# Optimization experiments

Hardware: AMD Instinct MI355X
Metric: run time of the kernel (lower is better)

The kernel has to match this reference:

```python
import jax, jax.numpy as jnp
import numpy as np

HIDDEN = 2048
INTER = 768
NUM_EXPERTS = 32
TOP_K = 8
B, S = 1, 512


def setup_inputs() -> dict:
    key = jax.random.key(0)
    ks = jax.random.split(key, 5)
    scale_h = 1.0 / np.sqrt(HIDDEN)
    scale_i = 1.0 / np.sqrt(INTER)
    return {
        "hidden_states": jax.random.normal(ks[0], (B, S, HIDDEN), dtype=jnp.float32),
        # router gate: nn.Linear(hidden, num_experts), weight [E, H]
        "gate_w": jax.random.normal(ks[1], (NUM_EXPERTS, HIDDEN), dtype=jnp.float32) * scale_h,
        # stacked expert weights, already transposed for x @ W as in setup_tt: [E, H, I] / [E, I, H]
        "gate_proj": jax.random.normal(ks[2], (NUM_EXPERTS, HIDDEN, INTER), dtype=jnp.float32) * scale_h,
        "up_proj": jax.random.normal(ks[3], (NUM_EXPERTS, HIDDEN, INTER), dtype=jnp.float32) * scale_h,
        "down_proj": jax.random.normal(ks[4], (NUM_EXPERTS, INTER, HIDDEN), dtype=jnp.float32) * scale_i,
    }


def reference(hidden_states, gate_w, gate_proj, up_proj, down_proj):
    b, s, h = hidden_states.shape
    x = hidden_states.reshape(-1, h)                      # [T, H]
    t = x.shape[0]

    # --- routing: softmax over experts -> top-k -> renormalize (norm_topk_prob=True) ---
    router_logits = x @ gate_w.T                          # [T, E]
    probs = jax.nn.softmax(router_logits, axis=-1)
    top_w, top_i = jax.lax.top_k(probs, TOP_K)            # [T, K]
    top_w = top_w / jnp.sum(top_w, axis=-1, keepdims=True)

    # dense combine weights [T, E]; top-k indices are distinct per token
    comb = jnp.zeros((t, NUM_EXPERTS), dtype=x.dtype)
    comb = comb.at[jnp.arange(t)[:, None], top_i].add(top_w)

    # --- expert GLU MLPs (all experts, combine-masked; same math as dispatch/combine) ---
    g = jnp.einsum('th,ehi->eti', x, gate_proj)           # [E, T, I]
    u = jnp.einsum('th,ehi->eti', x, up_proj)             # [E, T, I]
    glu = jax.nn.silu(g) * u                              # [E, T, I]
    o = jnp.einsum('eti,eih->eth', glu, down_proj)        # [E, T, H]

    # weighted combine over experts
    y = jnp.einsum('eth,te->th', o, comb)                 # [T, H]
    return y.reshape(b, s, h)
```

## Files before the change

### kernel.cpp

```cpp
#include <hip/hip_runtime.h>
#include <math.h>

#define H 2048
#define I 768
#define NE 32
#define TOPK 8
#define T 512

typedef __attribute__((ext_vector_type(4))) float f32x4;
typedef __attribute__((ext_vector_type(8))) short s16x8;

#define WS_TOPW_OFF    1024
#define WS_ENTRIES_OFF (1024 + 16384)
#define WS_XB_OFF      131072
#define WS_GLU_OFF     (4*1024*1024)

__device__ __forceinline__ unsigned int f2bf(float f) {
    unsigned int u = __float_as_uint(f);
    return (u + 0x7FFFu + ((u >> 16) & 1u)) >> 16;
}

__global__ __launch_bounds__(256) void convert_x_kernel(
    const float* __restrict__ x, ushort* __restrict__ xb)
{
    int i = (blockIdx.x * 256 + threadIdx.x) * 8;
    float4 a = *(const float4*)(x + i);
    float4 b = *(const float4*)(x + i + 4);
    uint4 o;
    o.x = f2bf(a.x) | (f2bf(a.y) << 16);
    o.y = f2bf(a.z) | (f2bf(a.w) << 16);
    o.z = f2bf(b.x) | (f2bf(b.y) << 16);
    o.w = f2bf(b.z) | (f2bf(b.w) << 16);
    *(uint4*)(xb + i) = o;
}

__global__ __launch_bounds__(256) void router_kernel(
    const float* __restrict__ x, const float* __restrict__ gw,
    float* __restrict__ topw, int* __restrict__ counts, int* __restrict__ entries)
{
    int t = blockIdx.x;
    const float* xt = x + (size_t)t * H;
    __shared__ float logits[NE];

    int e   = threadIdx.x >> 3;
    int sub = threadIdx.x & 7;
    const float* we = gw + (size_t)e * H;
    float acc = 0.f;
    for (int h = sub; h < H; h += 8) acc += xt[h] * we[h];
    acc += __shfl_down(acc, 4);
    acc += __shfl_down(acc, 2);
    acc += __shfl_down(acc, 1);
    if (sub == 0) logits[e] = acc;
    __syncthreads();

    if (threadIdx.x == 0) {
        float l[NE];
        #pragma unroll
        for (int i2 = 0; i2 < NE; ++i2) l[i2] = logits[i2];
        int bi[TOPK]; float bv[TOPK];
        for (int k = 0; k < TOPK; ++k) {
            float best = -1e30f; int b = 0;
            for (int i2 = 0; i2 < NE; ++i2)
                if (l[i2] > best) { best = l[i2]; b = i2; }
            bi[k] = b; bv[k] = best; l[b] = -1e30f;
        }
        float m = bv[0], s = 0.f, w[TOPK];
        for (int k = 0; k < TOPK; ++k) { w[k] = expf(bv[k] - m); s += w[k]; }
        float inv = 1.f / s;
        for (int k = 0; k < TOPK; ++k) {
            int p = t * TOPK + k;
            topw[p] = w[k] * inv;
            int pos = atomicAdd(&counts[bi[k]], 1);
            entries[bi[k] * T + pos] = p;
        }
    }
}

__global__ __launch_bounds__(256) void gateup_kernel(
    const ushort* __restrict__ xb, const float* __restrict__ Wg, const float* __restrict__ Wu,
    const int* __restrict__ counts, const int* __restrict__ entries,
    ushort* __restrict__ glu)
{
    int e  = blockIdx.x;
    int nt = blockIdx.y;
    int mt = blockIdx.z;
    int n  = counts[e];
    if (mt * 128 >= n) return;

    __shared__ ushort A_lds[128 * 72];
    __shared__ ushort Bg_lds[64 * 72];
    __shared__ ushort Bu_lds[64 * 72];
    __shared__ int prow[128];

    int tid = threadIdx.x;
    if (tid < 128) {
        int idx = mt * 128 + tid;
        prow[tid] = (idx < n) ? entries[e * T + idx] : -1;
    }
    __syncthreads();

    int lane = tid & 63;
    int wid  = tid >> 6;
    int wm = wid >> 1, wn = wid & 1;
    int quad = lane >> 4, l16 = lane & 15;

    f32x4 accg[4][2], accu[4][2];
    #pragma unroll
    for (int mi = 0; mi < 4; ++mi)
        #pragma unroll
        for (int ni = 0; ni < 2; ++ni) {
            #pragma unroll
            for (int r = 0; r < 4; ++r) { accg[mi][ni][r] = 0.f; accu[mi][ni][r] = 0.f; }
        }

    const float* wgB = Wg + (size_t)e * H * I + nt * 64;
    const float* wuB = Wu + (size_t)e * H * I + nt * 64;
    int n4 = tid & 15;
    int kb = tid >> 4;

    for (int hc = 0; hc < H; hc += 64) {
        #pragma unroll
        for (int s = 0; s < 4; ++s) {
            int c = tid + s * 256;
            int r = c >> 3, ch = c & 7;
            int p = prow[r];
            int4 v = make_int4(0, 0, 0, 0);
            if (p >= 0)
                v = *(const int4*)(xb + (size_t)(p >> 3) * H + hc + ch * 8);
            *(int4*)&A_lds[r * 72 + ch * 8] = v;
        }
        #pragma unroll
        for (int q = 0; q < 2; ++q) {
            int k = kb * 2 + q * 32;
            const float* g0 = wgB + (size_t)(hc + k) * I + n4 * 4;
            const float* u0 = wuB + (size_t)(hc + k) * I + n4 * 4;
            float4 ga = *(const float4*)g0;
            float4 gb = *(const float4*)(g0 + I);
            float4 ua = *(const float4*)u0;
            float4 ub = *(const float4*)(u0 + I);
            float gax[4] = {ga.x, ga.y, ga.z, ga.w};
            float gbx[4] = {gb.x, gb.y, gb.z, gb.w};
            float uax[4] = {ua.x, ua.y, ua.z, ua.w};
            float ubx[4] = {ub.x, ub.y, ub.z, ub.w};
            #pragma unroll
            for (int i2 = 0; i2 < 4; ++i2) {
                *(unsigned int*)&Bg_lds[(n4 * 4 + i2) * 72 + k] = f2bf(gax[i2]) | (f2bf(gbx[i2]) << 16);
                *(unsigned int*)&Bu_lds[(n4 * 4 + i2) * 72 + k] = f2bf(uax[i2]) | (f2bf(ubx[i2]) << 16);
            }
        }
        __syncthreads();
        #pragma unroll
        for (int s = 0; s < 2; ++s) {
            int ko = s * 32 + quad * 8;
            s16x8 af[4];
            #pragma unroll
            for (int mi = 0; mi < 4; ++mi)
                af[mi] = *(const s16x8*)&A_lds[(wm * 64 + mi * 16 + l16) * 72 + ko];
            #pragma unroll
            for (int ni = 0; ni < 2; ++ni) {
                s16x8 bg = *(const s16x8*)&Bg_lds[(wn * 32 + ni * 16 + l16) * 72 + ko];
                s16x8 bu = *(const s16x8*)&Bu_lds[(wn * 32 + ni * 16 + l16) * 72 + ko];
                #pragma unroll
                for (int mi = 0; mi < 4; ++mi) {
                    accg[mi][ni] = __builtin_amdgcn_mfma_f32_16x16x32_bf16(af[mi], bg, accg[mi][ni], 0, 0, 0);
                    accu[mi][ni] = __builtin_amdgcn_mfma_f32_16x16x32_bf16(af[mi], bu, accu[mi][ni], 0, 0, 0);
                }
            }
        }
        __syncthreads();
    }

    #pragma unroll
    for (int mi = 0; mi < 4; ++mi) {
        #pragma unroll
        for (int reg = 0; reg < 4; ++reg) {
            int r = wm * 64 + mi * 16 + quad * 4 + reg;
            int p = prow[r];
            if (p >= 0) {
                size_t base = (size_t)p * I + nt * 64 + wn * 32;
                #pragma unroll
                for (int ni = 0; ni < 2; ++ni) {
                    float g = accg[mi][ni][reg];
                    float u = accu[mi][ni][reg];
                    float sv = g / (1.f + __expf(-g)) * u;
                    glu[base + ni * 16 + l16] = (ushort)f2bf(sv);
                }
            }
        }
    }
}

__global__ __launch_bounds__(256) void down_kernel(
    const ushort* __restrict__ glu, const float* __restrict__ Wd,
    const int* __restrict__ counts, const int* __restrict__ entries,
    const float* __restrict__ topw, float* __restrict__ out)
{
    int e  = blockIdx.x;
    int nt = blockIdx.y;
    int mt = blockIdx.z;
    int n  = counts[e];
    if (mt * 128 >= n) return;

    __shared__ ushort A_lds[128 * 72];
    __shared__ ushort B_lds[64 * 72];
    __shared__ int   prow[128];
    __shared__ float pw[128];

    int tid = threadIdx.x;
    if (tid < 128) {
        int idx = mt * 128 + tid;
        int p = (idx < n) ? entries[e * T + idx] : -1;
        prow[tid] = p;
        pw[tid]   = (p >= 0) ? topw[p] : 0.f;
    }
    __syncthreads();

    int lane = tid & 63;
    int wid  = tid >> 6;
    int wm = wid >> 1, wn = wid & 1;
    int quad = lane >> 4, l16 = lane & 15;

    f32x4 acc[4][2];
    #pragma unroll
    for (int mi = 0; mi < 4; ++mi)
        #pragma unroll
        for (int ni = 0; ni < 2; ++ni) {
            #pragma unroll
            for (int r = 0; r < 4; ++r) acc[mi][ni][r] = 0.f;
        }

    const float* wdB = Wd + (size_t)e * I * H + nt * 64;
    int n4 = tid & 15;
    int kb = tid >> 4;

    for (int kc = 0; kc < I; kc += 64) {
        #pragma unroll
        for (int s = 0; s < 4; ++s) {
            int c = tid + s * 256;
            int r = c >> 3, ch = c & 7;
            int p = prow[r];
            int4 v = make_int4(0, 0, 0, 0);
            if (p >= 0)
                v = *(const int4*)(glu + (size_t)p * I + kc + ch * 8);
            *(int4*)&A_lds[r * 72 + ch * 8] = v;
        }
        #pragma unroll
        for (int q = 0; q < 2; ++q) {
            int k = kb * 2 + q * 32;
            const float* d0 = wdB + (size_t)(kc + k) * H + n4 * 4;
            float4 da = *(const float4*)d0;
            float4 db = *(const float4*)(d0 + H);
            float dax[4] = {da.x, da.y, da.z, da.w};
            float dbx[4] = {db.x, db.y, db.z, db.w};
            #pragma unroll
            for (int i2 = 0; i2 < 4; ++i2)
                *(unsigned int*)&B_lds[(n4 * 4 + i2) * 72 + k] = f2bf(dax[i2]) | (f2bf(dbx[i2]) << 16);
        }
        __syncthreads();
        #pragma unroll
        for (int s = 0; s < 2; ++s) {
            int ko = s * 32 + quad * 8;
            s16x8 af[4];
            #pragma unroll
            for (int mi = 0; mi < 4; ++mi)
                af[mi] = *(const s16x8*)&A_lds[(wm * 64 + mi * 16 + l16) * 72 + ko];
            #pragma unroll
            for (int ni = 0; ni < 2; ++ni) {
                s16x8 bf = *(const s16x8*)&B_lds[(wn * 32 + ni * 16 + l16) * 72 + ko];
                #pragma unroll
                for (int mi = 0; mi < 4; ++mi)
                    acc[mi][ni] = __builtin_amdgcn_mfma_f32_16x16x32_bf16(af[mi], bf, acc[mi][ni], 0, 0, 0);
            }
        }
        __syncthreads();
    }

    #pragma unroll
    for (int mi = 0; mi < 4; ++mi) {
        #pragma unroll
        for (int reg = 0; reg < 4; ++reg) {
            int r = wm * 64 + mi * 16 + quad * 4 + reg;
            int p = prow[r];
            if (p >= 0) {
                int tok = p >> 3;
                float wgt = pw[r];
                size_t base = (size_t)tok * H + nt * 64 + wn * 32;
                #pragma unroll
                for (int ni = 0; ni < 2; ++ni)
                    atomicAdd(&out[base + ni * 16 + l16], wgt * acc[mi][ni][reg]);
            }
        }
    }
}

extern "C" void kernel_launch(void* const* d_in, const int* in_sizes, int n_in,
                              void* d_out, int out_size, void* d_ws, size_t ws_size,
                              hipStream_t stream) {
    const float* x  = (const float*)d_in[0];
    const float* gw = (const float*)d_in[1];
    const float* Wg = (const float*)d_in[2];
    const float* Wu = (const float*)d_in[3];
    const float* Wd = (const float*)d_in[4];
    float* out = (float*)d_out;

    char* ws = (char*)d_ws;
    int*    counts  = (int*)ws;
    float*  topw    = (float*)(ws + WS_TOPW_OFF);
    int*    entries = (int*)(ws + WS_ENTRIES_OFF);
    ushort* xb      = (ushort*)(ws + WS_XB_OFF);
    ushort* glu     = (ushort*)(ws + WS_GLU_OFF);

    hipMemsetAsync(d_ws, 0, 1024, stream);
    hipMemsetAsync(d_out, 0, (size_t)out_size * sizeof(float), stream);

    convert_x_kernel<<<T * H / (256 * 8), 256, 0, stream>>>(x, xb);
    router_kernel<<<T, 256, 0, stream>>>(x, gw, topw, counts, entries);

    dim3 g2(NE, I / 64, 4);
    gateup_kernel<<<g2, 256, 0, stream>>>(xb, Wg, Wu, counts, entries, glu);

    dim3 g3(NE, H / 64, 4);
    down_kernel<<<g3, 256, 0, stream>>>(glu, Wd, counts, entries, topw, out);
}
```

Baseline: 684.8 us.

## Software-pipeline expert GEMMs with async global-to-LDS loads and double-buffered A

After: 686.5 us. About the same (+0.3%).

```diff
diff --git a/kernel.cpp b/kernel.cpp
--- a/kernel.cpp
+++ b/kernel.cpp
@@ -18,6 +18,11 @@
 __device__ __forceinline__ unsigned int f2bf(float f) {
     unsigned int u = __float_as_uint(f);
     return (u + 0x7FFFu + ((u >> 16) & 1u)) >> 16;
+}
+__device__ __forceinline__ unsigned int cvtpk(float lo, float hi) {
+    unsigned int r;
+    asm("v_cvt_pk_bf16_f32 %0, %1, %2" : "=v"(r) : "v"(lo), "v"(hi));
+    return r;
 }
 
 __global__ __launch_bounds__(256) void convert_x_kernel(
@@ -27,10 +32,10 @@
     float4 a = *(const float4*)(x + i);
     float4 b = *(const float4*)(x + i + 4);
     uint4 o;
-    o.x = f2bf(a.x) | (f2bf(a.y) << 16);
-    o.y = f2bf(a.z) | (f2bf(a.w) << 16);
-    o.z = f2bf(b.x) | (f2bf(b.y) << 16);
-    o.w = f2bf(b.z) | (f2bf(b.w) << 16);
+    o.x = cvtpk(a.x, a.y);
+    o.y = cvtpk(a.z, a.w);
+    o.z = cvtpk(b.x, b.y);
+    o.w = cvtpk(b.z, b.w);
     *(uint4*)(xb + i) = o;
 }
 
@@ -87,7 +92,7 @@
     int n  = counts[e];
     if (mt * 128 >= n) return;
 
-    __shared__ ushort A_lds[128 * 72];
+    __shared__ ushort A_lds[2][128 * 64];
     __shared__ ushort Bg_lds[64 * 72];
     __shared__ ushort Bu_lds[64 * 72];
     __shared__ int prow[128];
@@ -104,6 +109,44 @@
     int wm = wid >> 1, wn = wid & 1;
     int quad = lane >> 4, l16 = lane & 15;
 
+    const ushort* asrc[4];
+    #pragma unroll
+    for (int j = 0; j < 4; ++j) {
+        int r = (wid * 4 + j) * 8 + (lane >> 3);
+        int c = (lane & 7) ^ (r & 7);
+        int p = prow[r]; if (p < 0) p = 0;
+        asrc[j] = xb + (size_t)(p >> 3) * H + c * 8;
+    }
+
+    int n4 = tid & 15, kb = tid >> 4;
+    const float* pg = Wg + (size_t)e * H * I + (size_t)(kb * 2) * I + nt * 64 + n4 * 4;
+    const float* pu = Wu + (size_t)e * H * I + (size_t)(kb * 2) * I + nt * 64 + n4 * 4;
+    float4 bg[2][2], bu[2][2];
+
+    int bofs[2][4];
+    #pragma unroll
+    for (int q = 0; q < 2; ++q)
+        #pragma unroll
+        for (int i2 = 0; i2 < 4; ++i2) {
+            int r = n4 * 4 + i2, d = kb + 16 * q;
+            bofs[q][i2] = r * 72 + (((d >> 2) ^ ((r >> 3) & 7)) << 3) + ((d & 3) << 1);
+        }
+    int aofs[2][4], brofs[2][2];
+    #pragma unroll
+    for (int s = 0; s < 2; ++s) {
+        int g = 4 * s + quad;
+        #pragma unroll
+        for (int mi = 0; mi < 4; ++mi) {
+            int R = wm * 64 + mi * 16 + l16;
+            aofs[s][mi] = R * 64 + ((g ^ (R & 7)) << 3);
+        }
+        #pragma unroll
+        for (int ni = 0; ni < 2; ++ni) {
+            int R = wn * 32 + ni * 16 + l16;
+            brofs[s][ni] = R * 72 + ((g ^ ((R >> 3) & 7)) << 3);
+        }
+    }
+
     f32x4 accg[4][2], accu[4][2];
     #pragma unroll
     for (int mi = 0; mi < 4; ++mi)
@@ -113,61 +156,67 @@
             for (int r = 0; r < 4; ++r) { accg[mi][ni][r] = 0.f; accu[mi][ni][r] = 0.f; }
         }
 
-    const float* wgB = Wg + (size_t)e * H * I + nt * 64;
-    const float* wuB = Wu + (size_t)e * H * I + nt * 64;
-    int n4 = tid & 15;
-    int kb = tid >> 4;
-
-    for (int hc = 0; hc < H; hc += 64) {
-        #pragma unroll
-        for (int s = 0; s < 4; ++s) {
-            int c = tid + s * 256;
-            int r = c >> 3, ch = c & 7;
-            int p = prow[r];
-            int4 v = make_int4(0, 0, 0, 0);
-            if (p >= 0)
-                v = *(const int4*)(xb + (size_t)(p >> 3) * H + hc + ch * 8);
-            *(int4*)&A_lds[r * 72 + ch * 8] = v;
-        }
+    auto issue_a = [&](int bi2, int hc) {
+        #pragma unroll
+        for (int j = 0; j < 4; ++j)
+            __builtin_amdgcn_global_load_lds(
+                (const __attribute__((address_space(1))) void*)(asrc[j] + hc),
+                (__attribute__((address_space(3))) void*)(&A_lds[bi2][(wid * 4 + j) * 512]),
+                16, 0, 0);
+    };
+    auto load_b = [&]() {
         #pragma unroll
         for (int q = 0; q < 2; ++q) {
-            int k = kb * 2 + q * 32;
-            const float* g0 = wgB + (size_t)(hc + k) * I + n4 * 4;
-            const float* u0 = wuB + (size_t)(hc + k) * I + n4 * 4;
-            float4 ga = *(const float4*)g0;
-            float4 gb = *(const float4*)(g0 + I);
-            float4 ua = *(const float4*)u0;
-            float4 ub = *(const float4*)(u0 + I);
-            float gax[4] = {ga.x, ga.y, ga.z, ga.w};
-            float gbx[4] = {gb.x, gb.y, gb.z, gb.w};
-            float uax[4] = {ua.x, ua.y, ua.z, ua.w};
-            float ubx[4] = {ub.x, ub.y, ub.z, ub.w};
+            const float* g0 = pg + (size_t)(32 * q) * I;
+            const float* u0 = pu + (size_t)(32 * q) * I;
+            bg[q][0] = *(const float4*)g0; bg[q][1] = *(const float4*)(g0 + I);
+            bu[q][0] = *(const float4*)u0; bu[q][1] = *(const float4*)(u0 + I);
+        }
+        pg += 64 * I; pu += 64 * I;
+    };
+    auto store_b = [&]() {
+        #pragma unroll
+        for (int q = 0; q < 2; ++q) {
+            const float* gl = (const float*)&bg[q][0];
+            const float* gh = (const float*)&bg[q][1];
+            const float* ul = (const float*)&bu[q][0];
+            const float* uh = (const float*)&bu[q][1];
             #pragma unroll
             for (int i2 = 0; i2 < 4; ++i2) {
-                *(unsigned int*)&Bg_lds[(n4 * 4 + i2) * 72 + k] = f2bf(gax[i2]) | (f2bf(gbx[i2]) << 16);
-                *(unsigned int*)&Bu_lds[(n4 * 4 + i2) * 72 + k] = f2bf(uax[i2]) | (f2bf(ubx[i2]) << 16);
+                *(unsigned int*)&Bg_lds[bofs[q][i2]] = cvtpk(gl[i2], gh[i2]);
+                *(unsigned int*)&Bu_lds[bofs[q][i2]] = cvtpk(ul[i2], uh[i2]);
             }
         }
-        __syncthreads();
+    };
+
+    issue_a(0, 0);
+    load_b();
+
+    for (int it = 0; it < H / 64; ++it) {
+        __builtin_amdgcn_s_barrier();
+        if (it + 1 < H / 64) issue_a((it + 1) & 1, (it + 1) * 64);
+        store_b();
+        if (it + 1 < H / 64) load_b();
+        asm volatile("s_waitcnt lgkmcnt(0) vmcnt(12)" ::: "memory");
+        __builtin_amdgcn_sched_barrier(0);
+        __builtin_amdgcn_s_barrier();
+        const ushort* Ab = A_lds[it & 1];
         #pragma unroll
         for (int s = 0; s < 2; ++s) {
-            int ko = s * 32 + quad * 8;
             s16x8 af[4];
             #pragma unroll
-            for (int mi = 0; mi < 4; ++mi)
-                af[mi] = *(const s16x8*)&A_lds[(wm * 64 + mi * 16 + l16) * 72 + ko];
+            for (int mi = 0; mi < 4; ++mi) af[mi] = *(const s16x8*)&Ab[aofs[s][mi]];
             #pragma unroll
             for (int ni = 0; ni < 2; ++ni) {
-                s16x8 bg = *(const s16x8*)&Bg_lds[(wn * 32 + ni * 16 + l16) * 72 + ko];
-                s16x8 bu = *(const s16x8*)&Bu_lds[(wn * 32 + ni * 16 + l16) * 72 + ko];
+                s16x8 bgf  = *(const s16x8*)&Bg_lds[brofs[s][ni]];
+                s16x8 buf2 = *(const s16x8*)&Bu_lds[brofs[s][ni]];
                 #pragma unroll
                 for (int mi = 0; mi < 4; ++mi) {
-                    accg[mi][ni] = __builtin_amdgcn_mfma_f32_16x16x32_bf16(af[mi], bg, accg[mi][ni], 0, 0, 0);
-                    accu[mi][ni] = __builtin_amdgcn_mfma_f32_16x16x32_bf16(af[mi], bu, accu[mi][ni], 0, 0, 0);
+                    accg[mi][ni] = __builtin_amdgcn_mfma_f32_16x16x32_bf16(af[mi], bgf,  accg[mi][ni], 0, 0, 0);
+                    accu[mi][ni] = __builtin_amdgcn_mfma_f32_16x16x32_bf16(af[mi], buf2, accu[mi][ni], 0, 0, 0);
                 }
             }
         }
-        __syncthreads();
     }
 
     #pragma unroll
@@ -201,8 +250,8 @@
     int n  = counts[e];
     if (mt * 128 >= n) return;
 
-    __shared__ ushort A_lds[128 * 72];
-    __shared__ ushort B_lds[64 * 72];
+    __shared__ ushort A_lds[2][128 * 64];
+    __shared__ ushort Bd_lds[64 * 72];
     __shared__ int   prow[128];
     __shared__ float pw[128];
 
@@ -220,6 +269,43 @@
     int wm = wid >> 1, wn = wid & 1;
     int quad = lane >> 4, l16 = lane & 15;
 
+    const ushort* asrc[4];
+    #pragma unroll
+    for (int j = 0; j < 4; ++j) {
+        int r = (wid * 4 + j) * 8 + (lane >> 3);
+        int c = (lane & 7) ^ (r & 7);
+        int p = prow[r]; if (p < 0) p = 0;
+        asrc[j] = glu + (size_t)p * I + c * 8;
+    }
+
+    int n4 = tid & 15, kb = tid >> 4;
+    const float* pd = Wd + (size_t)e * I * H + (size_t)(kb * 2) * H + nt * 64 + n4 * 4;
+    float4 bd[2][2];
+
+    int bofs[2][4];
+    #pragma unroll
+    for (int q = 0; q < 2; ++q)
+        #pragma unroll
+        for (int i2 = 0; i2 < 4; ++i2) {
+            int r = n4 * 4 + i2, d = kb + 16 * q;
+            bofs[q][i2] = r * 72 + (((d >> 2) ^ ((r >> 3) & 7)) << 3) + ((d & 3) << 1);
+        }
+    int aofs[2][4], brofs[2][2];
+    #pragma unroll
+    for (int s = 0; s < 2; ++s) {
+        int g = 4 * s + quad;
+        #pragma unroll
+        for (int mi = 0; mi < 4; ++mi) {
+            int R = wm * 64 + mi * 16 + l16;
+            aofs[s][mi] = R * 64 + ((g ^ (R & 7)) << 3);
+        }
+        #pragma unroll
+        for (int ni = 0; ni < 2; ++ni) {
+            int R = wn * 32 + ni * 16 + l16;
+            brofs[s][ni] = R * 72 + ((g ^ ((R >> 3) & 7)) << 3);
+        }
+    }
+
     f32x4 acc[4][2];
     #pragma unroll
     for (int mi = 0; mi < 4; ++mi)
@@ -229,50 +315,58 @@
             for (int r = 0; r < 4; ++r) acc[mi][ni][r] = 0.f;
         }
 
-    const float* wdB = Wd + (size_t)e * I * H + nt * 64;
-    int n4 = tid & 15;
-    int kb = tid >> 4;
-
-    for (int kc = 0; kc < I; kc += 64) {
-        #pragma unroll
-        for (int s = 0; s < 4; ++s) {
-            int c = tid + s * 256;
-            int r = c >> 3, ch = c & 7;
-            int p = prow[r];
-            int4 v = make_int4(0, 0, 0, 0);
-            if (p >= 0)
-                v = *(const int4*)(glu + (size_t)p * I + kc + ch * 8);
-            *(int4*)&A_lds[r * 72 + ch * 8] = v;
-        }
+    auto issue_a = [&](int bi2, int kc) {
+        #pragma unroll
+        for (int j = 0; j < 4; ++j)
+            __builtin_amdgcn_global_load_lds(
+                (const __attribute__((address_space(1))) void*)(asrc[j] + kc),
+                (__attribute__((address_space(3))) void*)(&A_lds[bi2][(wid * 4 + j) * 512]),
+                16, 0, 0);
+    };
+    auto load_b = [&]() {
         #pragma unroll
         for (int q = 0; q < 2; ++q) {
-            int k = kb * 2 + q * 32;
-            const float* d0 = wdB + (size_t)(kc + k) * H + n4 * 4;
-            float4 da = *(const float4*)d0;
-            float4 db = *(const float4*)(d0 + H);
-            float dax[4] = {da.x, da.y, da.z, da.w};
-            float dbx[4] = {db.x, db.y, db.z, db.w};
+            const float* d0 = pd + (size_t)(32 * q) * H;
+            bd[q][0] = *(const float4*)d0; bd[q][1] = *(const float4*)(d0 + H);
+        }
+        pd += 64 * H;
+    };
+    auto store_b = [&]() {
+        #pragma unroll
+        for (int q = 0; q < 2; ++q) {
+            const float* dl = (const float*)&bd[q][0];
+            const float* dh = (const float*)&bd[q][1];
             #pragma unroll
             for (int i2 = 0; i2 < 4; ++i2)
-                *(unsigned int*)&B_lds[(n4 * 4 + i2) * 72 + k] = f2bf(dax[i2]) | (f2bf(dbx[i2]) << 16);
-        }
-        __syncthreads();
+                *(unsigned int*)&Bd_lds[bofs[q][i2]] = cvtpk(dl[i2], dh[i2]);
+        }
+    };
+
+    issue_a(0, 0);
+    load_b();
+
+    for (int it = 0; it < I / 64; ++it) {
+        __builtin_amdgcn_s_barrier();
+        if (it + 1 < I / 64) issue_a((it + 1) & 1, (it + 1) * 64);
+        store_b();
+        if (it + 1 < I / 64) load_b();
+        asm volatile("s_waitcnt lgkmcnt(0) vmcnt(8)" ::: "memory");
+        __builtin_amdgcn_sched_barrier(0);
+        __builtin_amdgcn_s_barrier();
+        const ushort* Ab = A_lds[it & 1];
         #pragma unroll
         for (int s = 0; s < 2; ++s) {
-            int ko = s * 32 + quad * 8;
             s16x8 af[4];
             #pragma unroll
-            for (int mi = 0; mi < 4; ++mi)
-                af[mi] = *(const s16x8*)&A_lds[(wm * 64 + mi * 16 + l16) * 72 + ko];
+            for (int mi = 0; mi < 4; ++mi) af[mi] = *(const s16x8*)&Ab[aofs[s][mi]];
             #pragma unroll
             for (int ni = 0; ni < 2; ++ni) {
-                s16x8 bf = *(const s16x8*)&B_lds[(wn * 32 + ni * 16 + l16) * 72 + ko];
+                s16x8 bf2 = *(const s16x8*)&Bd_lds[brofs[s][ni]];
                 #pragma unroll
                 for (int mi = 0; mi < 4; ++mi)
-                    acc[mi][ni] = __builtin_amdgcn_mfma_f32_16x16x32_bf16(af[mi], bf, acc[mi][ni], 0, 0, 0);
+                    acc[mi][ni] = __builtin_amdgcn_mfma_f32_16x16x32_bf16(af[mi], bf2, acc[mi][ni], 0, 0, 0);
             }
         }
-        __syncthreads();
     }
 
     #pragma unroll
```
